# Kernel tuning notes

Measured on AMD Instinct MI355X. Metric: run time of the kernel, lower is better.

## Reference

```python
import jax, jax.numpy as jnp
import numpy as np

TOPK = 5
LAMBDA_ALIGN_K = 16.0
MOM = 0.9          # EMA momentum
DEFAULT_SCORE = 0.5  # EMA bank default (bank starts empty)
EPS = 1e-8
NEG = 1.0e9


def pairwise_cosine(X):
    # torch F.normalize: X / max(||X||, eps)
    n = jnp.linalg.norm(X, axis=-1, keepdims=True)
    Xn = X / jnp.maximum(n, EPS)
    sim = Xn @ Xn.T
    return jnp.clip(sim, -1.0 + EPS, 1.0 - EPS)


def knn_mask(sim, allowed_base, topk=TOPK):
    B = sim.shape[0]
    eye = jnp.eye(B, dtype=sim.dtype)
    allowed = allowed_base * (1.0 - eye)
    masked = sim - NEG * eye
    masked = jnp.where(allowed < 0.5, -NEG, masked)
    masked = jnp.where(masked < 0.0, -NEG, masked)
    cand = (masked > 0).sum(axis=1)
    k = min(topk, max(B - 1, 1))
    keep_row = (cand >= topk).astype(sim.dtype)
    keep = keep_row[:, None] * keep_row[None, :]
    idx = jax.lax.top_k(masked, k)[1]                       # [B, k]
    M = jnp.zeros_like(sim).at[jnp.arange(B)[:, None], idx].set(1.0)
    M = jnp.maximum(M, M.T)
    return M * allowed * keep


def build_intra(sim, same, topk=TOPK):
    M = knn_mask(sim, same, topk)
    A = jnp.maximum(sim * M, 0.0) * same
    return A, M


def pga_loss(feats_sub, labels_sub):
    # feats_sub: [L, b, d]
    L = feats_sub.shape[0]
    same = (labels_sub[:, None] == labels_sub[None, :]).astype(jnp.float32)
    sims = jax.vmap(pairwise_cosine)(feats_sub)             # [L, b, b]
    A, M = jax.vmap(lambda s: build_intra(s, same))(sims)   # [L, b, b] each

    # EMA degree-based scores (no-grad in original; bank starts empty so
    # fetch-after-update == mom*default + (1-mom)*score_cur)
    S_intra = jnp.maximum(sims * same, 0.0)
    deg = jnp.maximum((S_intra > 0).sum(axis=2).astype(jnp.float32), 1.0)
    score_cur = jax.nn.sigmoid(S_intra.sum(axis=2) / deg)   # [L, b]
    ema = jax.lax.stop_gradient(MOM * DEFAULT_SCORE + (1.0 - MOM) * score_cur)

    # layer-pair masked MSE alignment, target detached
    A_deep = A[1:]
    A_tgt = jax.lax.stop_gradient(A[:-1])
    M_eff = jnp.maximum(M[:-1], M[1:])                      # [L-1, b, b]
    W = ema[:-1, :, None] * ema[:-1, None, :]               # [L-1, b, b]
    diff2 = (A_deep - A_tgt) ** 2 * W
    num = (diff2 * M_eff).sum(axis=(1, 2))
    den = jnp.maximum((M_eff * W).sum(axis=(1, 2)), EPS)
    terms = jnp.where(M_eff.sum(axis=(1, 2)) > 0, num / den, 0.0)
    raw = terms.sum() / max(L - 1, 1)
    return LAMBDA_ALIGN_K * raw


def setup_inputs() -> dict:
    key = jax.random.key(0)
    k1, k2 = jax.random.split(key)
    feats_final = jax.random.normal(k1, (8, 2048, 512), dtype=jnp.float32)
    labels = jax.random.randint(k2, (2048,), 0, 128).astype(jnp.int64)
    sample_ids = jnp.arange(2048, dtype=jnp.int64)
    return {"feats_final": feats_final, "labels": labels, "sample_ids": sample_ids}


def reference(feats_final, labels, sample_ids):
    # candidate subset from last layer (no-grad in original)
    X_last = feats_final[-1]
    S_last = pairwise_cosine(X_last)
    same_full = (labels[:, None] == labels[None, :]).astype(jnp.float32)
    _, M_last = build_intra(S_last, same_full)
    cand_mask = (M_last > 0).sum(axis=1) > 0
    idx_sub = jnp.nonzero(cand_mask)[0]  # eager (concrete) subselection
    feats_sub = feats_final[:, idx_sub]  # [L, b, d]
    labels_sub = labels[idx_sub]
    return pga_loss(feats_sub, labels_sub)
```

## Files before the change

### kernel.cpp

```cpp
#include <hip/hip_runtime.h>
#include <cmath>

#define NB   2048
#define ND   512
#define NL   8
#define NLAB 128
#define MAXM 64
#define TOPK_ 5
#define NTH  256
#define MAXSLOT 9
#define GSTRIDE (MAXM*MAXM)

__global__ __launch_bounds__(NTH) void k_gram(
    const float* __restrict__ feats, const int* __restrict__ labels,
    float* __restrict__ G, int* __restrict__ cnt)
{
    __shared__ int cnts[NTH];
    __shared__ int g_s[MAXM];
    __shared__ float Xt[MAXM][132];
    int c = blockIdx.x, l = blockIdx.y, tid = threadIdx.x;

    int my[8]; int n = 0; int base_i = tid * 8;
    for (int t = 0; t < 8; ++t) {
        int i = base_i + t;
        if (labels[i] == c) my[n++] = i;
    }
    cnts[tid] = n;
    __syncthreads();
    for (int off = 1; off < NTH; off <<= 1) {
        int v = (tid >= off) ? cnts[tid - off] : 0;
        __syncthreads();
        cnts[tid] += v;
        __syncthreads();
    }
    int excl = cnts[tid] - n;
    int m = cnts[NTH - 1]; if (m > MAXM) m = MAXM;
    for (int t = 0; t < n; ++t) {
        int slot = excl + t;
        if (slot < MAXM) g_s[slot] = my[t];
    }
    if (l == 0 && tid == 0) cnt[c] = m;
    __syncthreads();
    if (m == 0) return;

    const float* X = feats + (size_t)l * NB * ND;
    const int P = m * (m + 1) / 2;
    float acc0[MAXSLOT], acc1[MAXSLOT];
    short is_[MAXSLOT], js_[MAXSLOT];
    int ns = 0;
    for (int p = tid; p < P; p += NTH) {
        int i = (int)((sqrtf(8.0f * (float)p + 1.0f) - 1.0f) * 0.5f);
        while (((i + 1) * (i + 2)) / 2 <= p) ++i;
        while ((i * (i + 1)) / 2 > p) --i;
        is_[ns] = (short)i;
        js_[ns] = (short)(p - (i * (i + 1)) / 2);
        acc0[ns] = 0.0f; acc1[ns] = 0.0f;
        ++ns;
    }
    for (int kc = 0; kc < ND; kc += 128) {
        if (kc) __syncthreads();
        for (int idx = tid; idx < (m << 5); idx += NTH) {
            int i = idx >> 5, k4 = idx & 31;
            float4 v = *(const float4*)(X + ((size_t)g_s[i] << 9) + kc + (k4 << 2));
            *(float4*)&Xt[i][k4 << 2] = v;
        }
        __syncthreads();
        for (int s = 0; s < ns; ++s) {
            int i = is_[s], j = js_[s];
            float a0 = acc0[s], a1 = acc1[s];
            #pragma unroll
            for (int k4 = 0; k4 < 32; ++k4) {
                float4 a = *(const float4*)&Xt[i][k4 << 2];
                float4 b = *(const float4*)&Xt[j][k4 << 2];
                a0 = fmaf(a.x, b.x, a0); a1 = fmaf(a.y, b.y, a1);
                a0 = fmaf(a.z, b.z, a0); a1 = fmaf(a.w, b.w, a1);
            }
            acc0[s] = a0; acc1[s] = a1;
        }
    }
    float* Gc = G + ((size_t)l * NLAB + c) * GSTRIDE;
    for (int s = 0; s < ns; ++s) {
        int i = is_[s], j = js_[s];
        float v = acc0[s] + acc1[s];
        Gc[i * MAXM + j] = v;
        Gc[j * MAXM + i] = v;
    }
}

__device__ __forceinline__ void load_tile(
    const float* __restrict__ Gc, int m, int tid, float (*Gs)[65], float* rinv)
{
    if (tid < 64) rinv[tid] = (tid < m) ? 1.0f / fmaxf(sqrtf(Gc[tid * MAXM + tid]), 1e-8f) : 0.0f;
    __syncthreads();
    for (int idx = tid; idx < 4096; idx += NTH) {
        int i = idx >> 6, j = idx & 63;
        float raw = Gc[idx];
        float v = fminf(fmaxf(raw * rinv[i] * rinv[j], -1.0f), 1.0f);
        Gs[i][j] = (i < m && j < m) ? v : -2.0f;
    }
    __syncthreads();
}

__global__ __launch_bounds__(NTH) void k_phase1(
    const float* __restrict__ G, const int* __restrict__ cnt,
    unsigned long long* __restrict__ insub)
{
    __shared__ float Gs[64][65];
    __shared__ float rinv[64];
    __shared__ unsigned long long tops_s[64];
    __shared__ unsigned char keep_s[64];
    int c = blockIdx.x, tid = threadIdx.x;
    int m = cnt[c]; if (m > MAXM) m = MAXM;
    if (m == 0) { if (tid == 0) insub[c] = 0ull; return; }

    const float* Gc7 = G + ((size_t)7 * NLAB + c) * GSTRIDE;
    load_tile(Gc7, m, tid, Gs, rinv);
    if (tid < 64) { keep_s[tid] = 0; tops_s[tid] = 0ull; }
    __syncthreads();
    unsigned long long tops = 0ull; bool keep = false;
    if (tid < m) {
        float v0=-1.f,v1=-1.f,v2=-1.f,v3=-1.f,v4=-1.f;
        int i0=0,i1=0,i2=0,i3=0,i4=0, cand=0;
        #pragma unroll 8
        for (int j = 0; j < 64; ++j) {
            float v = Gs[tid][j];
            if (v > 0.0f && j != tid) {
                ++cand;
                if      (v > v0) { v4=v3;i4=i3; v3=v2;i3=i2; v2=v1;i2=i1; v1=v0;i1=i0; v0=v;i0=j; }
                else if (v > v1) { v4=v3;i4=i3; v3=v2;i3=i2; v2=v1;i2=i1; v1=v;i1=j; }
                else if (v > v2) { v4=v3;i4=i3; v3=v2;i3=i2; v2=v;i2=j; }
                else if (v > v3) { v4=v3;i4=i3; v3=v;i3=j; }
                else if (v > v4) { v4=v;i4=j; }
            }
        }
        keep = (cand >= TOPK_);
        if (keep) tops = (1ull<<i0)|(1ull<<i1)|(1ull<<i2)|(1ull<<i3)|(1ull<<i4);
        keep_s[tid] = keep ? 1 : 0; tops_s[tid] = tops;
    }
    __syncthreads();
    unsigned long long Mrow = 0ull;
    if (tid < m && keep) {
        for (int j = 0; j < 64; ++j) {
            if (j == tid || !keep_s[j]) continue;
            if (((tops >> j) & 1ull) || ((tops_s[j] >> tid) & 1ull)) Mrow |= (1ull << j);
        }
    }
    if (tid < 64) {
        unsigned long long b = __ballot(Mrow != 0ull);
        if (tid == 0) insub[c] = b;
    }
}

__global__ __launch_bounds__(NTH) void k_decide(
    const float* __restrict__ G, const int* __restrict__ cnt,
    const unsigned long long* __restrict__ insub,
    unsigned long long* __restrict__ Mbits, float* __restrict__ ema)
{
    __shared__ float Gs[64][65];
    __shared__ float rinv[64];
    __shared__ unsigned long long tops_s[64];
    __shared__ unsigned char keep_s[64];
    int c = blockIdx.x, l = blockIdx.y, tid = threadIdx.x;
    int m = cnt[c]; if (m > MAXM) m = MAXM;
    if (m == 0) return;
    unsigned long long sub = insub[c];

    const float* Gc = G + ((size_t)l * NLAB + c) * GSTRIDE;
    load_tile(Gc, m, tid, Gs, rinv);
    if (tid < 64) { keep_s[tid] = 0; tops_s[tid] = 0ull; }
    __syncthreads();
    unsigned long long tops = 0ull; bool keep = false; bool act = false;
    float emaval = 0.0f;
    if (tid < m) {
        act = (sub >> tid) & 1ull;
        if (act) {
            float v0=-1.f,v1=-1.f,v2=-1.f,v3=-1.f,v4=-1.f;
            int i0=0,i1=0,i2=0,i3=0,i4=0, cand=0, dg=0;
            float rs = 0.0f;
            #pragma unroll 8
            for (int j = 0; j < 64; ++j) {
                float v = Gs[tid][j];
                if (!((sub >> j) & 1ull)) v = -2.0f;
                if (v > 0.0f) {
                    rs += v; ++dg;
                    if (j != tid) {
                        ++cand;
                        if      (v > v0) { v4=v3;i4=i3; v3=v2;i3=i2; v2=v1;i2=i1; v1=v0;i1=i0; v0=v;i0=j; }
                        else if (v > v1) { v4=v3;i4=i3; v3=v2;i3=i2; v2=v1;i2=i1; v1=v;i1=j; }
                        else if (v > v2) { v4=v3;i4=i3; v3=v2;i3=i2; v2=v;i2=j; }
                        else if (v > v3) { v4=v3;i4=i3; v3=v;i3=j; }
                        else if (v > v4) { v4=v;i4=j; }
                    }
                }
            }
            keep = (cand >= TOPK_);
            if (keep) tops = (1ull<<i0)|(1ull<<i1)|(1ull<<i2)|(1ull<<i3)|(1ull<<i4);
            float deg = (float)(dg > 0 ? dg : 1);
            float score = 1.0f / (1.0f + expf(-rs / deg));
            emaval = 0.45f + 0.1f * score;
        }
        keep_s[tid] = keep ? 1 : 0; tops_s[tid] = tops;
    }
    __syncthreads();
    if (tid < m) {
        unsigned long long Mrow = 0ull;
        if (keep) {
            for (int j = 0; j < 64; ++j) {
                if (j == tid || !keep_s[j]) continue;
                if (((tops >> j) & 1ull) || ((tops_s[j] >> tid) & 1ull)) Mrow |= (1ull << j);
            }
        }
        Mbits[((size_t)l * NLAB + c) * MAXM + tid] = Mrow;
        ema[((size_t)l * NLAB + c) * MAXM + tid] = emaval;
    }
}

__global__ __launch_bounds__(NTH) void k_pairs(
    const float* __restrict__ G, const int* __restrict__ cnt,
    const unsigned long long* __restrict__ Mbits, const float* __restrict__ ema,
    float* __restrict__ partial)
{
    __shared__ float r0[64], r1[64];
    __shared__ unsigned long long M0s[64], M1s[64];
    __shared__ float es[64];
    __shared__ float red[12];
    int c = blockIdx.x, p = blockIdx.y, tid = threadIdx.x;
    int m = cnt[c]; if (m > MAXM) m = MAXM;
    const float* G0 = G + ((size_t)p       * NLAB + c) * GSTRIDE;
    const float* G1 = G + ((size_t)(p + 1) * NLAB + c) * GSTRIDE;
    if (tid < m) {
        M0s[tid] = Mbits[((size_t)p * NLAB + c) * MAXM + tid];
        M1s[tid] = Mbits[((size_t)(p + 1) * NLAB + c) * MAXM + tid];
        es[tid]  = ema[((size_t)p * NLAB + c) * MAXM + tid];
        r0[tid]  = 1.0f / fmaxf(sqrtf(G0[tid * MAXM + tid]), 1e-8f);
        r1[tid]  = 1.0f / fmaxf(sqrtf(G1[tid * MAXM + tid]), 1e-8f);
    }
    __syncthreads();
    float fn = 0.0f, fd = 0.0f, fc = 0.0f;
    for (int idx = tid; idx < (m << 6); idx += NTH) {
        int i = idx >> 6, j = idx & 63;
        if (j >= m) continue;
        bool b0 = (M0s[i] >> j) & 1ull;
        bool b1 = (M1s[i] >> j) & 1ull;
        if (b0 | b1) {
            float v0 = b0 ? fminf(fmaxf(G0[idx] * r0[i] * r0[j], -1.0f), 1.0f) : 0.0f;
            float v1 = b1 ? fminf(fmaxf(G1[idx] * r1[i] * r1[j], -1.0f), 1.0f) : 0.0f;
            float w = es[i] * es[j];
            float d = v1 - v0;
            fn = fmaf(d * d, w, fn);
            fd += w;
            fc += 1.0f;
        }
    }
    for (int off = 32; off > 0; off >>= 1) {
        fn += __shfl_down(fn, off);
        fd += __shfl_down(fd, off);
        fc += __shfl_down(fc, off);
    }
    int w = tid >> 6;
    if ((tid & 63) == 0) { red[w * 3] = fn; red[w * 3 + 1] = fd; red[w * 3 + 2] = fc; }
    __syncthreads();
    if (tid == 0) {
        float* dst = partial + ((size_t)p * NLAB + c) * 4;
        dst[0] = red[0] + red[3] + red[6] + red[9];
        dst[1] = red[1] + red[4] + red[7] + red[10];
        dst[2] = red[2] + red[5] + red[8] + red[11];
    }
}

__global__ void k_final(const float* __restrict__ partial, float* __restrict__ out)
{
    int tid = threadIdx.x;
    float total = 0.0f;
    for (int p = 0; p < NL - 1; ++p) {
        float n = 0.0f, d = 0.0f, cc = 0.0f;
        for (int c = tid; c < NLAB; c += 64) {
            const float* src = partial + ((size_t)p * NLAB + c) * 4;
            n += src[0]; d += src[1]; cc += src[2];
        }
        for (int off = 32; off > 0; off >>= 1) {
            n += __shfl_down(n, off);
            d += __shfl_down(d, off);
            cc += __shfl_down(cc, off);
        }
        if (tid == 0 && cc > 0.0f) total += n / fmaxf(d, 1e-8f);
    }
    if (tid == 0) out[0] = 16.0f * total / 7.0f;
}

extern "C" void kernel_launch(void* const* d_in, const int* in_sizes, int n_in,
                              void* d_out, int out_size, void* d_ws, size_t ws_size,
                              hipStream_t stream) {
    const float* feats  = (const float*)d_in[0];
    const int*   labels = (const int*)d_in[1];
    char* w = (char*)d_ws;
    size_t gbytes = (size_t)NL * NLAB * GSTRIDE * 4;
    float*    G       = (float*)(w);
    float*    partial = (float*)(w + gbytes);
    int*      cnt     = (int*)(w + gbytes + 14336);
    unsigned long long* insub = (unsigned long long*)(w + gbytes + 14848);
    unsigned long long* Mbits = (unsigned long long*)(w + gbytes + 16384);
    float*    ema     = (float*)(w + gbytes + 16384 + 524288);
    float*    out     = (float*)d_out;

    k_gram  <<<dim3(NLAB, NL), NTH, 0, stream>>>(feats, labels, G, cnt);
    k_phase1<<<NLAB, NTH, 0, stream>>>(G, cnt, insub);
    k_decide<<<dim3(NLAB, NL), NTH, 0, stream>>>(G, cnt, insub, Mbits, ema);
    k_pairs <<<dim3(NLAB, NL - 1), NTH, 0, stream>>>(G, cnt, Mbits, ema, partial);
    k_final <<<1, 64, 0, stream>>>(partial, out);
}
```

Measured before the change: 135.5 us.

## Fuse phase1, decide and pairs kernels into one per-class-per-pair kernel

Merges the candidate-subset kernel, the per-layer kNN decision kernel and the layer-pair loss kernel into a single kernel indexed by (class, layer pair). Each block recomputes the last-layer subset and the kNN masks for both of its layers from shared-memory tiles, so the Mbits, ema and insub global buffers and two kernel launches go away. In exchange it does redundant work: the phase-1 step is repeated by all seven pair blocks, and each middle layer's decision is computed twice.

```diff
diff --git a/kernel.cpp b/kernel.cpp
--- a/kernel.cpp
+++ b/kernel.cpp
@@ -101,72 +101,11 @@
     __syncthreads();
 }
 
-__global__ __launch_bounds__(NTH) void k_phase1(
-    const float* __restrict__ G, const int* __restrict__ cnt,
-    unsigned long long* __restrict__ insub)
-{
-    __shared__ float Gs[64][65];
-    __shared__ float rinv[64];
-    __shared__ unsigned long long tops_s[64];
-    __shared__ unsigned char keep_s[64];
-    int c = blockIdx.x, tid = threadIdx.x;
-    int m = cnt[c]; if (m > MAXM) m = MAXM;
-    if (m == 0) { if (tid == 0) insub[c] = 0ull; return; }
-
-    const float* Gc7 = G + ((size_t)7 * NLAB + c) * GSTRIDE;
-    load_tile(Gc7, m, tid, Gs, rinv);
-    if (tid < 64) { keep_s[tid] = 0; tops_s[tid] = 0ull; }
-    __syncthreads();
-    unsigned long long tops = 0ull; bool keep = false;
-    if (tid < m) {
-        float v0=-1.f,v1=-1.f,v2=-1.f,v3=-1.f,v4=-1.f;
-        int i0=0,i1=0,i2=0,i3=0,i4=0, cand=0;
-        #pragma unroll 8
-        for (int j = 0; j < 64; ++j) {
-            float v = Gs[tid][j];
-            if (v > 0.0f && j != tid) {
-                ++cand;
-                if      (v > v0) { v4=v3;i4=i3; v3=v2;i3=i2; v2=v1;i2=i1; v1=v0;i1=i0; v0=v;i0=j; }
-                else if (v > v1) { v4=v3;i4=i3; v3=v2;i3=i2; v2=v1;i2=i1; v1=v;i1=j; }
-                else if (v > v2) { v4=v3;i4=i3; v3=v2;i3=i2; v2=v;i2=j; }
-                else if (v > v3) { v4=v3;i4=i3; v3=v;i3=j; }
-                else if (v > v4) { v4=v;i4=j; }
-            }
-        }
-        keep = (cand >= TOPK_);
-        if (keep) tops = (1ull<<i0)|(1ull<<i1)|(1ull<<i2)|(1ull<<i3)|(1ull<<i4);
-        keep_s[tid] = keep ? 1 : 0; tops_s[tid] = tops;
-    }
-    __syncthreads();
-    unsigned long long Mrow = 0ull;
-    if (tid < m && keep) {
-        for (int j = 0; j < 64; ++j) {
-            if (j == tid || !keep_s[j]) continue;
-            if (((tops >> j) & 1ull) || ((tops_s[j] >> tid) & 1ull)) Mrow |= (1ull << j);
-        }
-    }
-    if (tid < 64) {
-        unsigned long long b = __ballot(Mrow != 0ull);
-        if (tid == 0) insub[c] = b;
-    }
-}
-
-__global__ __launch_bounds__(NTH) void k_decide(
-    const float* __restrict__ G, const int* __restrict__ cnt,
-    const unsigned long long* __restrict__ insub,
-    unsigned long long* __restrict__ Mbits, float* __restrict__ ema)
-{
-    __shared__ float Gs[64][65];
-    __shared__ float rinv[64];
-    __shared__ unsigned long long tops_s[64];
-    __shared__ unsigned char keep_s[64];
-    int c = blockIdx.x, l = blockIdx.y, tid = threadIdx.x;
-    int m = cnt[c]; if (m > MAXM) m = MAXM;
-    if (m == 0) return;
-    unsigned long long sub = insub[c];
-
-    const float* Gc = G + ((size_t)l * NLAB + c) * GSTRIDE;
-    load_tile(Gc, m, tid, Gs, rinv);
+__device__ __forceinline__ void decide_layer(
+    const float (*Gs)[65], int m, int tid, unsigned long long sub,
+    unsigned long long* tops_s, unsigned char* keep_s,
+    unsigned long long* Mb, float* es, bool want_ema)
+{
     if (tid < 64) { keep_s[tid] = 0; tops_s[tid] = 0ull; }
     __syncthreads();
     unsigned long long tops = 0ull; bool keep = false; bool act = false;
@@ -195,57 +134,107 @@
             }
             keep = (cand >= TOPK_);
             if (keep) tops = (1ull<<i0)|(1ull<<i1)|(1ull<<i2)|(1ull<<i3)|(1ull<<i4);
-            float deg = (float)(dg > 0 ? dg : 1);
-            float score = 1.0f / (1.0f + expf(-rs / deg));
-            emaval = 0.45f + 0.1f * score;
+            if (want_ema) {
+                float deg = (float)(dg > 0 ? dg : 1);
+                float score = 1.0f / (1.0f + expf(-rs / deg));
+                emaval = 0.45f + 0.1f * score;
+            }
         }
         keep_s[tid] = keep ? 1 : 0; tops_s[tid] = tops;
     }
     __syncthreads();
-    if (tid < m) {
+    if (tid < 64) {
         unsigned long long Mrow = 0ull;
-        if (keep) {
+        if (tid < m && keep) {
             for (int j = 0; j < 64; ++j) {
                 if (j == tid || !keep_s[j]) continue;
                 if (((tops >> j) & 1ull) || ((tops_s[j] >> tid) & 1ull)) Mrow |= (1ull << j);
             }
         }
-        Mbits[((size_t)l * NLAB + c) * MAXM + tid] = Mrow;
-        ema[((size_t)l * NLAB + c) * MAXM + tid] = emaval;
-    }
-}
-
-__global__ __launch_bounds__(NTH) void k_pairs(
+        Mb[tid] = Mrow;
+        if (want_ema) es[tid] = emaval;
+    }
+    __syncthreads();
+}
+
+__global__ __launch_bounds__(NTH) void k_main(
     const float* __restrict__ G, const int* __restrict__ cnt,
-    const unsigned long long* __restrict__ Mbits, const float* __restrict__ ema,
     float* __restrict__ partial)
 {
-    __shared__ float r0[64], r1[64];
-    __shared__ unsigned long long M0s[64], M1s[64];
-    __shared__ float es[64];
+    __shared__ float Gs0[64][65];
+    __shared__ float Gs1[64][65];
+    __shared__ float rinv[64];
+    __shared__ unsigned long long tops_s[64];
+    __shared__ unsigned char keep_s[64];
+    __shared__ unsigned long long Mb0[64], Mb1[64];
+    __shared__ float es0[64];
+    __shared__ unsigned long long insub_sh;
     __shared__ float red[12];
     int c = blockIdx.x, p = blockIdx.y, tid = threadIdx.x;
     int m = cnt[c]; if (m > MAXM) m = MAXM;
-    const float* G0 = G + ((size_t)p       * NLAB + c) * GSTRIDE;
-    const float* G1 = G + ((size_t)(p + 1) * NLAB + c) * GSTRIDE;
-    if (tid < m) {
-        M0s[tid] = Mbits[((size_t)p * NLAB + c) * MAXM + tid];
-        M1s[tid] = Mbits[((size_t)(p + 1) * NLAB + c) * MAXM + tid];
-        es[tid]  = ema[((size_t)p * NLAB + c) * MAXM + tid];
-        r0[tid]  = 1.0f / fmaxf(sqrtf(G0[tid * MAXM + tid]), 1e-8f);
-        r1[tid]  = 1.0f / fmaxf(sqrtf(G1[tid * MAXM + tid]), 1e-8f);
-    }
-    __syncthreads();
+    if (m == 0) {
+        if (tid == 0) {
+            float* dst = partial + ((size_t)p * NLAB + c) * 4;
+            dst[0] = 0.0f; dst[1] = 0.0f; dst[2] = 0.0f;
+        }
+        return;
+    }
+
+    load_tile(G + ((size_t)7 * NLAB + c) * GSTRIDE, m, tid, Gs0, rinv);
+    if (tid < 64) { keep_s[tid] = 0; tops_s[tid] = 0ull; }
+    __syncthreads();
+    {
+        unsigned long long tops = 0ull; bool keep = false;
+        if (tid < m) {
+            float v0=-1.f,v1=-1.f,v2=-1.f,v3=-1.f,v4=-1.f;
+            int i0=0,i1=0,i2=0,i3=0,i4=0, cand=0;
+            #pragma unroll 8
+            for (int j = 0; j < 64; ++j) {
+                float v = Gs0[tid][j];
+                if (v > 0.0f && j != tid) {
+                    ++cand;
+                    if      (v > v0) { v4=v3;i4=i3; v3=v2;i3=i2; v2=v1;i2=i1; v1=v0;i1=i0; v0=v;i0=j; }
+                    else if (v > v1) { v4=v3;i4=i3; v3=v2;i3=i2; v2=v1;i2=i1; v1=v;i1=j; }
+                    else if (v > v2) { v4=v3;i4=i3; v3=v2;i3=i2; v2=v;i2=j; }
+                    else if (v > v3) { v4=v3;i4=i3; v3=v;i3=j; }
+                    else if (v > v4) { v4=v;i4=j; }
+                }
+            }
+            keep = (cand >= TOPK_);
+            if (keep) tops = (1ull<<i0)|(1ull<<i1)|(1ull<<i2)|(1ull<<i3)|(1ull<<i4);
+            keep_s[tid] = keep ? 1 : 0; tops_s[tid] = tops;
+        }
+        __syncthreads();
+        unsigned long long Mrow = 0ull;
+        if (tid < m && keep) {
+            for (int j = 0; j < 64; ++j) {
+                if (j == tid || !keep_s[j]) continue;
+                if (((tops >> j) & 1ull) || ((tops_s[j] >> tid) & 1ull)) Mrow |= (1ull << j);
+            }
+        }
+        if (tid < 64) {
+            unsigned long long b = __ballot(Mrow != 0ull);
+            if (tid == 0) insub_sh = b;
+        }
+        __syncthreads();
+    }
+    unsigned long long sub = insub_sh;
+
+    load_tile(G + ((size_t)p       * NLAB + c) * GSTRIDE, m, tid, Gs0, rinv);
+    load_tile(G + ((size_t)(p + 1) * NLAB + c) * GSTRIDE, m, tid, Gs1, rinv);
+    decide_layer(Gs0, m, tid, sub, tops_s, keep_s, Mb0, es0, true);
+    decide_layer(Gs1, m, tid, sub, tops_s, keep_s, Mb1, es0, false);
+
     float fn = 0.0f, fd = 0.0f, fc = 0.0f;
     for (int idx = tid; idx < (m << 6); idx += NTH) {
         int i = idx >> 6, j = idx & 63;
         if (j >= m) continue;
-        bool b0 = (M0s[i] >> j) & 1ull;
-        bool b1 = (M1s[i] >> j) & 1ull;
+        bool b0 = (Mb0[i] >> j) & 1ull;
+        bool b1 = (Mb1[i] >> j) & 1ull;
         if (b0 | b1) {
-            float v0 = b0 ? fminf(fmaxf(G0[idx] * r0[i] * r0[j], -1.0f), 1.0f) : 0.0f;
-            float v1 = b1 ? fminf(fmaxf(G1[idx] * r1[i] * r1[j], -1.0f), 1.0f) : 0.0f;
-            float w = es[i] * es[j];
+            float v0 = b0 ? Gs0[i][j] : 0.0f;
+            float v1 = b1 ? Gs1[i][j] : 0.0f;
+            float w = es0[i] * es0[j];
             float d = v1 - v0;
             fn = fmaf(d * d, w, fn);
             fd += w;
@@ -298,14 +287,9 @@
     float*    G       = (float*)(w);
     float*    partial = (float*)(w + gbytes);
     int*      cnt     = (int*)(w + gbytes + 14336);
-    unsigned long long* insub = (unsigned long long*)(w + gbytes + 14848);
-    unsigned long long* Mbits = (unsigned long long*)(w + gbytes + 16384);
-    float*    ema     = (float*)(w + gbytes + 16384 + 524288);
     float*    out     = (float*)d_out;
 
-    k_gram  <<<dim3(NLAB, NL), NTH, 0, stream>>>(feats, labels, G, cnt);
-    k_phase1<<<NLAB, NTH, 0, stream>>>(G, cnt, insub);
-    k_decide<<<dim3(NLAB, NL), NTH, 0, stream>>>(G, cnt, insub, Mbits, ema);
-    k_pairs <<<dim3(NLAB, NL - 1), NTH, 0, stream>>>(G, cnt, Mbits, ema, partial);
-    k_final <<<1, 64, 0, stream>>>(partial, out);
-}
+    k_gram <<<dim3(NLAB, NL), NTH, 0, stream>>>(feats, labels, G, cnt);
+    k_main <<<dim3(NLAB, NL - 1), NTH, 0, stream>>>(G, cnt, partial);
+    k_final<<<1, 64, 0, stream>>>(partial, out);
+}
```

New measurement: 146.8 us. 8.4% more time.
